# Kernel optimization log

Measured on AMD Instinct MI355X. Metric: run time of the kernel, lower is better.

Reference implementation:

```python
import jax, jax.numpy as jnp
import numpy as np

SORB = 64
S = SORB // 2          # 32 pair-sites
D = 64                 # d_model
H = 8                  # n_heads
L = 6                  # n_layers
ALPHA = 16
BETA = 16
NEG = -1e30


def _ln(x, g, b, eps=1e-5):
    m = jnp.mean(x, -1, keepdims=True)
    v = jnp.mean((x - m) ** 2, -1, keepdims=True)
    return (x - m) * jax.lax.rsqrt(v + eps) * g + b


def setup_inputs() -> dict:
    key = jax.random.key(0)
    ks = jax.random.split(key, 16)
    B = 8192
    # valid +/-1 configurations: exactly ALPHA ups (even cols) and BETA downs (odd cols)
    su = jax.random.uniform(ks[0], (B, S))
    sd = jax.random.uniform(ks[1], (B, S))
    thr_u = jnp.sort(su, 1)[:, ALPHA - 1:ALPHA]
    thr_d = jnp.sort(sd, 1)[:, BETA - 1:BETA]
    up = (su <= thr_u).astype(jnp.float32)
    dn = (sd <= thr_d).astype(jnp.float32)
    x = (jnp.stack([up, dn], -1).reshape(B, SORB) * 2.0 - 1.0).astype(jnp.float32)
    sc = 0.02
    inp = {
        'x': x,
        'tok_emb': jax.random.normal(ks[2], (5, D), jnp.float32) * sc,
        'pos_emb': jax.random.normal(ks[3], (S, D), jnp.float32) * sc,
        'ln1_g': jnp.ones((L, D), jnp.float32), 'ln1_b': jnp.zeros((L, D), jnp.float32),
        'wqkv': jax.random.normal(ks[4], (L, D, 3 * D), jnp.float32) * sc,
        'bqkv': jnp.zeros((L, 3 * D), jnp.float32),
        'wo': jax.random.normal(ks[5], (L, D, D), jnp.float32) * sc,
        'bo': jnp.zeros((L, D), jnp.float32),
        'ln2_g': jnp.ones((L, D), jnp.float32), 'ln2_b': jnp.zeros((L, D), jnp.float32),
        'w1': jax.random.normal(ks[6], (L, D, 4 * D), jnp.float32) * sc,
        'b1': jnp.zeros((L, 4 * D), jnp.float32),
        'w2': jax.random.normal(ks[7], (L, 4 * D, D), jnp.float32) * sc,
        'b2': jnp.zeros((L, D), jnp.float32),
        'lnf_g': jnp.ones((D,), jnp.float32), 'lnf_b': jnp.zeros((D,), jnp.float32),
        'w_out': jax.random.normal(ks[8], (D, 4), jnp.float32) * sc,
        'b_out': jnp.zeros((4,), jnp.float32),
        'wp1': jax.random.normal(ks[9], (SORB, 64), jnp.float32) * sc,
        'bp1': jnp.zeros((64,), jnp.float32),
        'wp2': jax.random.normal(ks[10], (64, 64), jnp.float32) * sc,
        'bp2': jnp.zeros((64,), jnp.float32),
        'wp3': jax.random.normal(ks[11], (64, 1), jnp.float32) * sc,
        'bp3': jnp.zeros((1,), jnp.float32),
    }
    return inp


def _forward(x, tok_emb, pos_emb, ln1_g, ln1_b, wqkv, bqkv, wo, bo, ln2_g, ln2_b,
             w1, b1, w2, b2, lnf_g, lnf_b, w_out, b_out, wp1, bp1, wp2, bp2, wp3, bp3):
    B = x.shape[0]
    xb = ((x + 1.0) * 0.5).astype(jnp.int32)          # 0/1 occupations
    u = xb[:, 0::2]                                   # [B,S] up occ per pair
    dn = xb[:, 1::2]                                  # [B,S] down occ per pair
    pair_idx = u + 2 * dn                             # state_to_int: 0..3
    # amp input: pad token 4 then first S-1 pair codes (teacher-forced decoder)
    tokens = jnp.concatenate([jnp.full((B, 1), 4, jnp.int32), pair_idx[:, :S - 1]], 1)
    h = tok_emb[tokens] + pos_emb[None, :, :]
    hd = D // H
    causal = jnp.tril(jnp.ones((S, S), bool))
    for l in range(L):
        a = _ln(h, ln1_g[l], ln1_b[l])
        qkv = a @ wqkv[l] + bqkv[l]
        q, k, v = jnp.split(qkv, 3, -1)
        q = q.reshape(B, S, H, hd); k = k.reshape(B, S, H, hd); v = v.reshape(B, S, H, hd)
        scores = jnp.einsum('bshd,bthd->bhst', q, k) / np.sqrt(hd).astype(np.float32)
        att = jax.nn.softmax(jnp.where(causal, scores, NEG), -1)
        o = jnp.einsum('bhst,bthd->bshd', att, v).reshape(B, S, D)
        h = h + o @ wo[l] + bo[l]
        a = _ln(h, ln2_g[l], ln2_b[l])
        h = h + jax.nn.relu(a @ w1[l] + b1[l]) @ w2[l] + b2[l]
    logits = _ln(h, lnf_g, lnf_b) @ w_out + b_out     # [B,S,4]
    # symmetry mask: Fock -> FCI space (particle-number constraints per spin)
    nup = jnp.cumsum(u, 1) - u                        # exclusive prefix counts
    ndn = jnp.cumsum(dn, 1) - dn
    rem = (S - 1) - jnp.arange(S)                     # pairs remaining after this one
    du = jnp.array([0, 1, 0, 1], jnp.int32)           # option order: empty, a, b, full
    dd = jnp.array([0, 0, 1, 1], jnp.int32)
    nu = nup[..., None] + du
    nd = ndn[..., None] + dd                          # [B,S,4]
    r = rem[None, :, None]
    mask = (nu <= ALPHA) & (nd <= BETA) & (ALPHA - nu <= r) & (BETA - nd <= r)
    lp = jax.nn.log_softmax(jnp.where(mask, logits, NEG), -1)
    amps_log = jnp.take_along_axis(lp, pair_idx[..., None], 2)[..., 0].sum(1)  # [B]
    # phase MLP on the raw +/-1 configuration
    ph = jax.nn.relu(x @ wp1 + bp1)
    ph = jax.nn.relu(ph @ wp2 + bp2)
    ph = (ph @ wp3 + bp3).reshape(-1)
    return jnp.exp(1j * ph) * jnp.exp(0.5 * amps_log)  # complex wavefunction [B]


def reference(x, tok_emb, pos_emb, ln1_g, ln1_b, wqkv, bqkv, wo, bo, ln2_g, ln2_b,
              w1, b1, w2, b2, lnf_g, lnf_b, w_out, b_out, wp1, bp1, wp2, bp2, wp3, bp3):
    return _forward(x, tok_emb, pos_emb, ln1_g, ln1_b, wqkv, bqkv, wo, bo, ln2_g, ln2_b,
                    w1, b1, w2, b2, lnf_g, lnf_b, w_out, b_out, wp1, bp1, wp2, bp2, wp3, bp3)
```

## Files before the change

kernel.cpp:

```cpp
#include <hip/hip_runtime.h>

#define NEGV -1e30f
#define STR 36

__device__ __forceinline__ float4 ld4(const float* p) {
  return *reinterpret_cast<const float4*>(p);
}

__device__ __forceinline__ void fma8(float (&acc)[8], float4 w0, float4 w1, float a) {
  acc[0] = fmaf(a, w0.x, acc[0]);
  acc[1] = fmaf(a, w0.y, acc[1]);
  acc[2] = fmaf(a, w0.z, acc[2]);
  acc[3] = fmaf(a, w0.w, acc[3]);
  acc[4] = fmaf(a, w1.x, acc[4]);
  acc[5] = fmaf(a, w1.y, acc[5]);
  acc[6] = fmaf(a, w1.z, acc[6]);
  acc[7] = fmaf(a, w1.w, acc[7]);
}

__launch_bounds__(256, 2)
__global__ void dwf_kernel(
    const float* __restrict__ x,
    const float* __restrict__ tok_emb,
    const float* __restrict__ pos_emb,
    const float* __restrict__ ln1_g, const float* __restrict__ ln1_b,
    const float* __restrict__ wqkv,  const float* __restrict__ bqkv,
    const float* __restrict__ wo,    const float* __restrict__ bo,
    const float* __restrict__ ln2_g, const float* __restrict__ ln2_b,
    const float* __restrict__ w1,    const float* __restrict__ b1,
    const float* __restrict__ w2,    const float* __restrict__ b2,
    const float* __restrict__ lnf_g, const float* __restrict__ lnf_b,
    const float* __restrict__ w_out, const float* __restrict__ b_out,
    const float* __restrict__ wp1,   const float* __restrict__ bp1,
    const float* __restrict__ wp2,   const float* __restrict__ bp2,
    const float* __restrict__ wp3,   const float* __restrict__ bp3,
    float* __restrict__ out, int out_pairs, int nB)
{
  const int s2   = blockIdx.x;
  const int tid  = threadIdx.x;
  const int w    = tid >> 6;
  const int lane = tid & 63;
  const int i32  = tid & 31;
  const int hh   = tid >> 5;
  const int g    = (tid >> 5) & 1;
  const bool valid1 = (2 * s2 + 1) < nB;

  __shared__ float SA0[64 * STR], SA1[64 * STR];
  __shared__ float SB0[64 * STR], SB1[64 * STR];
  __shared__ float xs[128], phb[128];
  __shared__ int   pis[64], toks[64];

  const float* xbase = x + s2 * 128;
  if (tid < 128) xs[tid] = (tid < 64 || valid1) ? xbase[tid] : 0.f;

  unsigned long long um = 0ull, dm = 0ull;
  if (w < 2) {
    int ub = 0, db = 0;
    if (lane < 32 && (w == 0 || valid1)) {
      const float* xr = xbase + 64 * w;
      ub = xr[2 * i32]     > 0.f;
      db = xr[2 * i32 + 1] > 0.f;
    }
    um = __ballot(ub);
    dm = __ballot(db);
    int pi   = ub + 2 * db;
    int prev = __shfl_up(pi, 1);
    if (lane < 32) {
      pis[32 * w + i32]  = pi;
      toks[32 * w + i32] = (i32 == 0) ? 4 : prev;
    }
  }
  __syncthreads();

  float h0[8], h1[8];
  #pragma unroll
  for (int q = 0; q < 8; ++q) {
    int r = 8 * w + q;
    float pe = pos_emb[r * 64 + lane];
    h0[q] = tok_emb[toks[r] * 64 + lane]      + pe;
    h1[q] = tok_emb[toks[32 + r] * 64 + lane] + pe;
  }

  auto layernorm2 = [&](const float* gp, const float* bp) {
    float gv = gp[lane], bv = bp[lane];
    float va[8], vb[8];
    #pragma unroll
    for (int q = 0; q < 8; ++q) {
      float sa = h0[q], qa_ = h0[q] * h0[q];
      float sb = h1[q], qb_ = h1[q] * h1[q];
      #pragma unroll
      for (int off = 32; off; off >>= 1) {
        sa  += __shfl_xor(sa, off);
        qa_ += __shfl_xor(qa_, off);
        sb  += __shfl_xor(sb, off);
        qb_ += __shfl_xor(qb_, off);
      }
      float ma = sa * 0.015625f, mb = sb * 0.015625f;
      float ra = rsqrtf(fmaf(-ma, ma, qa_ * 0.015625f) + 1e-5f);
      float rb = rsqrtf(fmaf(-mb, mb, qb_ * 0.015625f) + 1e-5f);
      va[q] = fmaf((h0[q] - ma) * ra, gv, bv);
      vb[q] = fmaf((h1[q] - mb) * rb, gv, bv);
    }
    *reinterpret_cast<float4*>(&SA0[lane * STR + 8 * w])     = make_float4(va[0], va[1], va[2], va[3]);
    *reinterpret_cast<float4*>(&SA0[lane * STR + 8 * w + 4]) = make_float4(va[4], va[5], va[6], va[7]);
    *reinterpret_cast<float4*>(&SA1[lane * STR + 8 * w])     = make_float4(vb[0], vb[1], vb[2], vb[3]);
    *reinterpret_cast<float4*>(&SA1[lane * STR + 8 * w + 4]) = make_float4(vb[4], vb[5], vb[6], vb[7]);
  };

  for (int l = 0; l < 6; ++l) {
    layernorm2(ln1_g + l * 64, ln1_b + l * 64);
    __syncthreads();

    const float* wl = wqkv + l * 64 * 192;
    const float* bq = bqkv + l * 192;
    float qa0[8], qa1[8];
    #pragma unroll
    for (int e = 0; e < 8; ++e) { qa0[e] = bq[8 * hh + e]; qa1[e] = qa0[e]; }
    float kb = bq[64 + lane], vbb = bq[128 + lane];
    float k0a[8], k1a[8], v0a[8], v1a[8];
    #pragma unroll
    for (int q = 0; q < 8; ++q) { k0a[q] = kb; k1a[q] = kb; v0a[q] = vbb; v1a[q] = vbb; }

    #pragma unroll 2
    for (int d = 0; d < 64; ++d) {
      const float* wr = wl + d * 192;
      float4 wq0 = ld4(wr + 8 * hh);
      float4 wq1 = ld4(wr + 8 * hh + 4);
      float  wk  = wr[64 + lane];
      float  wv  = wr[128 + lane];
      float  av0 = SA0[d * STR + i32];
      float  av1 = SA1[d * STR + i32];
      float4 a0l = ld4(&SA0[d * STR + 8 * w]);
      float4 a0h = ld4(&SA0[d * STR + 8 * w + 4]);
      float4 a1l = ld4(&SA1[d * STR + 8 * w]);
      float4 a1h = ld4(&SA1[d * STR + 8 * w + 4]);
      fma8(qa0, wq0, wq1, av0);
      fma8(qa1, wq0, wq1, av1);
      fma8(k0a, a0l, a0h, wk);
      fma8(k1a, a1l, a1h, wk);
      fma8(v0a, a0l, a0h, wv);
      fma8(v1a, a1l, a1h, wv);
    }
    #pragma unroll
    for (int e = 0; e < 8; ++e) {
      qa0[e] *= 0.35355339059327373f;
      qa1[e] *= 0.35355339059327373f;
    }
    __syncthreads();

    *reinterpret_cast<float4*>(&SA0[lane * STR + 8 * w])     = make_float4(k0a[0], k0a[1], k0a[2], k0a[3]);
    *reinterpret_cast<float4*>(&SA0[lane * STR + 8 * w + 4]) = make_float4(k0a[4], k0a[5], k0a[6], k0a[7]);
    *reinterpret_cast<float4*>(&SA1[lane * STR + 8 * w])     = make_float4(k1a[0], k1a[1], k1a[2], k1a[3]);
    *reinterpret_cast<float4*>(&SA1[lane * STR + 8 * w + 4]) = make_float4(k1a[4], k1a[5], k1a[6], k1a[7]);
    *reinterpret_cast<float4*>(&SB0[lane * STR + 8 * w])     = make_float4(v0a[0], v0a[1], v0a[2], v0a[3]);
    *reinterpret_cast<float4*>(&SB0[lane * STR + 8 * w + 4]) = make_float4(v0a[4], v0a[5], v0a[6], v0a[7]);
    *reinterpret_cast<float4*>(&SB1[lane * STR + 8 * w])     = make_float4(v1a[0], v1a[1], v1a[2], v1a[3]);
    *reinterpret_cast<float4*>(&SB1[lane * STR + 8 * w + 4]) = make_float4(v1a[4], v1a[5], v1a[6], v1a[7]);
    __syncthreads();

    {
      float p[32];
      #pragma unroll
      for (int j4 = 0; j4 < 8; ++j4) {
        float a0 = 0.f, a1 = 0.f, a2 = 0.f, a3 = 0.f;
        #pragma unroll
        for (int c = 0; c < 8; ++c) {
          float4 kv = ld4(&SA0[(8 * hh + c) * STR + 4 * j4]);
          a0 = fmaf(qa0[c], kv.x, a0);
          a1 = fmaf(qa0[c], kv.y, a1);
          a2 = fmaf(qa0[c], kv.z, a2);
          a3 = fmaf(qa0[c], kv.w, a3);
        }
        p[4 * j4]     = a0;
        p[4 * j4 + 1] = a1;
        p[4 * j4 + 2] = a2;
        p[4 * j4 + 3] = a3;
      }
      float mx = NEGV;
      #pragma unroll
      for (int j = 0; j < 32; ++j) {
        p[j] = (j <= i32) ? p[j] : NEGV;
        mx = fmaxf(mx, p[j]);
      }
      float sum = 0.f;
      #pragma unroll
      for (int j = 0; j < 32; ++j) {
        p[j] = __expf(p[j] - mx);
        sum += p[j];
      }
      float inv = 1.0f / sum;
      #pragma unroll
      for (int e = 0; e < 8; ++e) {
        float acc = 0.f;
        #pragma unroll
        for (int j4 = 0; j4 < 8; ++j4) {
          float4 vv = ld4(&SB0[(8 * hh + e) * STR + 4 * j4]);
          acc = fmaf(p[4 * j4],     vv.x, acc);
          acc = fmaf(p[4 * j4 + 1], vv.y, acc);
          acc = fmaf(p[4 * j4 + 2], vv.z, acc);
          acc = fmaf(p[4 * j4 + 3], vv.w, acc);
        }
        SA0[(8 * hh + e) * STR + i32] = acc * inv;
      }
    }
    {
      float p[32];
      #pragma unroll
      for (int j4 = 0; j4 < 8; ++j4) {
        float a0 = 0.f, a1 = 0.f, a2 = 0.f, a3 = 0.f;
        #pragma unroll
        for (int c = 0; c < 8; ++c) {
          float4 kv = ld4(&SA1[(8 * hh + c) * STR + 4 * j4]);
          a0 = fmaf(qa1[c], kv.x, a0);
          a1 = fmaf(qa1[c], kv.y, a1);
          a2 = fmaf(qa1[c], kv.z, a2);
          a3 = fmaf(qa1[c], kv.w, a3);
        }
        p[4 * j4]     = a0;
        p[4 * j4 + 1] = a1;
        p[4 * j4 + 2] = a2;
        p[4 * j4 + 3] = a3;
      }
      float mx = NEGV;
      #pragma unroll
      for (int j = 0; j < 32; ++j) {
        p[j] = (j <= i32) ? p[j] : NEGV;
        mx = fmaxf(mx, p[j]);
      }
      float sum = 0.f;
      #pragma unroll
      for (int j = 0; j < 32; ++j) {
        p[j] = __expf(p[j] - mx);
        sum += p[j];
      }
      float inv = 1.0f / sum;
      #pragma unroll
      for (int e = 0; e < 8; ++e) {
        float acc = 0.f;
        #pragma unroll
        for (int j4 = 0; j4 < 8; ++j4) {
          float4 vv = ld4(&SB1[(8 * hh + e) * STR + 4 * j4]);
          acc = fmaf(p[4 * j4],     vv.x, acc);
          acc = fmaf(p[4 * j4 + 1], vv.y, acc);
          acc = fmaf(p[4 * j4 + 2], vv.z, acc);
          acc = fmaf(p[4 * j4 + 3], vv.w, acc);
        }
        SA1[(8 * hh + e) * STR + i32] = acc * inv;
      }
    }
    __syncthreads();

    const float* wop = wo + l * 4096 + lane;
    #pragma unroll 2
    for (int d = 0; d < 64; ++d) {
      float wv = wop[d * 64];
      float4 o0l = ld4(&SA0[d * STR + 8 * w]);
      float4 o0h = ld4(&SA0[d * STR + 8 * w + 4]);
      float4 o1l = ld4(&SA1[d * STR + 8 * w]);
      float4 o1h = ld4(&SA1[d * STR + 8 * w + 4]);
      fma8(h0, o0l, o0h, wv);
      fma8(h1, o1l, o1h, wv);
    }
    {
      float bov = bo[l * 64 + lane];
      #pragma unroll
      for (int q = 0; q < 8; ++q) { h0[q] += bov; h1[q] += bov; }
    }

    layernorm2(ln2_g + l * 64, ln2_b + l * 64);
    const float* w1base = w1 + l * 64 * 256;
    const float* w2base = w2 + l * 256 * 64;
    for (int cc = 0; cc < 4; ++cc) {
      float b1v = b1[l * 256 + cc * 64 + lane];
      float m0[8], m1v[8];
      #pragma unroll
      for (int q = 0; q < 8; ++q) { m0[q] = b1v; m1v[q] = b1v; }
      const float* w1p = w1base + cc * 64 + lane;
      #pragma unroll 2
      for (int d = 0; d < 64; ++d) {
        float wv = w1p[d * 256];
        float4 a0l = ld4(&SA0[d * STR + 8 * w]);
        float4 a0h = ld4(&SA0[d * STR + 8 * w + 4]);
        float4 a1l = ld4(&SA1[d * STR + 8 * w]);
        float4 a1h = ld4(&SA1[d * STR + 8 * w + 4]);
        fma8(m0,  a0l, a0h, wv);
        fma8(m1v, a1l, a1h, wv);
      }
      *reinterpret_cast<float4*>(&SB0[lane * STR + 8 * w]) =
          make_float4(fmaxf(m0[0], 0.f), fmaxf(m0[1], 0.f),
                      fmaxf(m0[2], 0.f), fmaxf(m0[3], 0.f));
      *reinterpret_cast<float4*>(&SB0[lane * STR + 8 * w + 4]) =
          make_float4(fmaxf(m0[4], 0.f), fmaxf(m0[5], 0.f),
                      fmaxf(m0[6], 0.f), fmaxf(m0[7], 0.f));
      *reinterpret_cast<float4*>(&SB1[lane * STR + 8 * w]) =
          make_float4(fmaxf(m1v[0], 0.f), fmaxf(m1v[1], 0.f),
                      fmaxf(m1v[2], 0.f), fmaxf(m1v[3], 0.f));
      *reinterpret_cast<float4*>(&SB1[lane * STR + 8 * w + 4]) =
          make_float4(fmaxf(m1v[4], 0.f), fmaxf(m1v[5], 0.f),
                      fmaxf(m1v[6], 0.f), fmaxf(m1v[7], 0.f));
      const float* w2p = w2base + cc * 64 * 64 + lane;
      #pragma unroll 2
      for (int dc = 0; dc < 64; ++dc) {
        float wv = w2p[dc * 64];
        float4 q0l = ld4(&SB0[dc * STR + 8 * w]);
        float4 q0h = ld4(&SB0[dc * STR + 8 * w + 4]);
        float4 q1l = ld4(&SB1[dc * STR + 8 * w]);
        float4 q1h = ld4(&SB1[dc * STR + 8 * w + 4]);
        fma8(h0, q0l, q0h, wv);
        fma8(h1, q1l, q1h, wv);
      }
    }
    {
      float b2v = b2[l * 64 + lane];
      #pragma unroll
      for (int q = 0; q < 8; ++q) { h0[q] += b2v; h1[q] += b2v; }
    }
  }

  layernorm2(lnf_g, lnf_b);
  __syncthreads();

  if (w < 2) {
    const float* SAt = w ? SA1 : SA0;
    float la = b_out[2 * g], lb = b_out[2 * g + 1];
    #pragma unroll 4
    for (int d = 0; d < 64; ++d) {
      float av = SAt[d * STR + i32];
      la = fmaf(av, w_out[d * 4 + 2 * g],     la);
      lb = fmaf(av, w_out[d * 4 + 2 * g + 1], lb);
    }
    float lc  = __shfl_xor(la, 32);
    float ldt = __shfl_xor(lb, 32);

    int r   = i32;
    int nup = __popcll(um & ((1ull << r) - 1ull));
    int ndn = __popcll(dm & ((1ull << r) - 1ull));
    int rem = 31 - r;
    float lg[4] = {la, lb, lc, ldt};
    float ml[4];
    #pragma unroll
    for (int c = 0; c < 4; ++c) {
      int nu = nup + (c & 1);
      int nd = ndn + (c >> 1);
      bool ok = (nu <= 16) && (nd <= 16) && (16 - nu <= rem) && (16 - nd <= rem);
      ml[c] = ok ? lg[c] : NEGV;
    }
    float m4 = fmaxf(fmaxf(ml[0], ml[1]), fmaxf(ml[2], ml[3]));
    float se = __expf(ml[0] - m4) + __expf(ml[1] - m4) +
               __expf(ml[2] - m4) + __expf(ml[3] - m4);
    int c = pis[32 * w + r];
    float mls = (c == 0) ? ml[0] : (c == 1) ? ml[1] : (c == 2) ? ml[2] : ml[3];
    float amps = (lane < 32) ? (mls - m4 - __logf(se)) : 0.f;
    #pragma unroll
    for (int off = 32; off; off >>= 1) amps += __shfl_xor(amps, off);

    const float* xst = xs + 64 * w;
    float p1 = bp1[lane];
    #pragma unroll 4
    for (int d = 0; d < 64; ++d)
      p1 = fmaf(xst[d], wp1[d * 64 + lane], p1);
    p1 = fmaxf(p1, 0.f);
    phb[64 * w + lane] = p1;
    float p2 = bp2[lane];
    #pragma unroll 4
    for (int d = 0; d < 64; ++d)
      p2 = fmaf(phb[64 * w + d], wp2[d * 64 + lane], p2);
    p2 = fmaxf(p2, 0.f);
    float p3 = p2 * wp3[lane];
    #pragma unroll
    for (int off = 32; off; off >>= 1) p3 += __shfl_xor(p3, off);
    float ph = p3 + bp3[0];

    if (lane == 0 && (w == 0 || valid1)) {
      int S = 2 * s2 + w;
      float amp = expf(0.5f * amps);
      if (out_pairs) {
        out[2 * S]     = amp * cosf(ph);
        out[2 * S + 1] = amp * sinf(ph);
      } else {
        out[S] = amp * cosf(ph);
      }
    }
  }
}

extern "C" void kernel_launch(void* const* d_in, const int* in_sizes, int n_in,
                              void* d_out, int out_size, void* d_ws, size_t ws_size,
                              hipStream_t stream) {
  (void)n_in; (void)d_ws; (void)ws_size;
  const int B = in_sizes[0] / 64;
  const int out_pairs = (out_size >= 2 * B) ? 1 : 0;
  const int grid = (B + 1) / 2;
  dwf_kernel<<<grid, 256, 0, stream>>>(
      (const float*)d_in[0],  (const float*)d_in[1],  (const float*)d_in[2],
      (const float*)d_in[3],  (const float*)d_in[4],  (const float*)d_in[5],
      (const float*)d_in[6],  (const float*)d_in[7],  (const float*)d_in[8],
      (const float*)d_in[9],  (const float*)d_in[10], (const float*)d_in[11],
      (const float*)d_in[12], (const float*)d_in[13], (const float*)d_in[14],
      (const float*)d_in[15], (const float*)d_in[16], (const float*)d_in[17],
      (const float*)d_in[18], (const float*)d_in[19], (const float*)d_in[20],
      (const float*)d_in[21], (const float*)d_in[22], (const float*)d_in[23],
      (const float*)d_in[24], (float*)d_out, out_pairs, B);
}
```

Measured before the change: 2.951 ms.

## Software-pipeline weight loads in GEMM loops and pair FFN chunk computation

Rewrites the QKV, output-projection, FFN1 and FFN2 inner loops so that global weight loads for the next group of rows are issued into double-buffered registers before the current group's FMAs run. This hides global-memory latency behind LDS reads and arithmetic. The FFN1 loop now computes two hidden chunks at once, so each shared-memory activation load is reused twice. The cost is higher register pressure, which under launch_bounds(256,2) could cause spills.

```diff
diff --git a/kernel.cpp b/kernel.cpp
--- a/kernel.cpp
+++ b/kernel.cpp
@@ -107,6 +107,40 @@
     *reinterpret_cast<float4*>(&SA1[lane * STR + 8 * w + 4]) = make_float4(vb[4], vb[5], vb[6], vb[7]);
   };
 
+  auto w2pass = [&](const float* w2p) {
+    float gA[8], gB[8];
+    #pragma unroll
+    for (int u = 0; u < 8; ++u) gA[u] = w2p[u * 64];
+    #pragma unroll 1
+    for (int dp = 0; dp < 4; ++dp) {
+      const int ds = dp * 16;
+      #pragma unroll
+      for (int u = 0; u < 8; ++u) gB[u] = w2p[((ds + 8 + u) & 63) * 64];
+      #pragma unroll
+      for (int u = 0; u < 8; ++u) {
+        const int dc = ds + u;
+        float4 q0l = ld4(&SB0[dc * STR + 8 * w]);
+        float4 q0h = ld4(&SB0[dc * STR + 8 * w + 4]);
+        float4 q1l = ld4(&SB1[dc * STR + 8 * w]);
+        float4 q1h = ld4(&SB1[dc * STR + 8 * w + 4]);
+        fma8(h0, q0l, q0h, gA[u]);
+        fma8(h1, q1l, q1h, gA[u]);
+      }
+      #pragma unroll
+      for (int u = 0; u < 8; ++u) gA[u] = w2p[((ds + 16 + u) & 63) * 64];
+      #pragma unroll
+      for (int u = 0; u < 8; ++u) {
+        const int dc = ds + 8 + u;
+        float4 q0l = ld4(&SB0[dc * STR + 8 * w]);
+        float4 q0h = ld4(&SB0[dc * STR + 8 * w + 4]);
+        float4 q1l = ld4(&SB1[dc * STR + 8 * w]);
+        float4 q1h = ld4(&SB1[dc * STR + 8 * w + 4]);
+        fma8(h0, q0l, q0h, gB[u]);
+        fma8(h1, q1l, q1h, gB[u]);
+      }
+    }
+  };
+
   for (int l = 0; l < 6; ++l) {
     layernorm2(ln1_g + l * 64, ln1_b + l * 64);
     __syncthreads();
@@ -121,25 +155,62 @@
     #pragma unroll
     for (int q = 0; q < 8; ++q) { k0a[q] = kb; k1a[q] = kb; v0a[q] = vbb; v1a[q] = vbb; }
 
-    #pragma unroll 2
-    for (int d = 0; d < 64; ++d) {
-      const float* wr = wl + d * 192;
-      float4 wq0 = ld4(wr + 8 * hh);
-      float4 wq1 = ld4(wr + 8 * hh + 4);
-      float  wk  = wr[64 + lane];
-      float  wv  = wr[128 + lane];
-      float  av0 = SA0[d * STR + i32];
-      float  av1 = SA1[d * STR + i32];
-      float4 a0l = ld4(&SA0[d * STR + 8 * w]);
-      float4 a0h = ld4(&SA0[d * STR + 8 * w + 4]);
-      float4 a1l = ld4(&SA1[d * STR + 8 * w]);
-      float4 a1h = ld4(&SA1[d * STR + 8 * w + 4]);
-      fma8(qa0, wq0, wq1, av0);
-      fma8(qa1, wq0, wq1, av1);
-      fma8(k0a, a0l, a0h, wk);
-      fma8(k1a, a1l, a1h, wk);
-      fma8(v0a, a0l, a0h, wv);
-      fma8(v1a, a1l, a1h, wv);
+    const float* wkp = wl + 64 + lane;
+    const float* wvp = wl + 128 + lane;
+    float kwA[4], vwA[4], kwB[4], vwB[4];
+    #pragma unroll
+    for (int u = 0; u < 4; ++u) { kwA[u] = wkp[u * 192]; vwA[u] = wvp[u * 192]; }
+    #pragma unroll 1
+    for (int dp = 0; dp < 8; ++dp) {
+      const int ds = dp * 8;
+      #pragma unroll
+      for (int u = 0; u < 4; ++u) {
+        const int dn = (ds + 4 + u) & 63;
+        kwB[u] = wkp[dn * 192]; vwB[u] = wvp[dn * 192];
+      }
+      #pragma unroll
+      for (int u = 0; u < 4; ++u) {
+        const int d = ds + u;
+        const float* wr = wl + d * 192;
+        float4 wq0 = ld4(wr + 8 * hh);
+        float4 wq1 = ld4(wr + 8 * hh + 4);
+        float  av0 = SA0[d * STR + i32];
+        float  av1 = SA1[d * STR + i32];
+        float4 a0l = ld4(&SA0[d * STR + 8 * w]);
+        float4 a0h = ld4(&SA0[d * STR + 8 * w + 4]);
+        float4 a1l = ld4(&SA1[d * STR + 8 * w]);
+        float4 a1h = ld4(&SA1[d * STR + 8 * w + 4]);
+        fma8(qa0, wq0, wq1, av0);
+        fma8(qa1, wq0, wq1, av1);
+        fma8(k0a, a0l, a0h, kwA[u]);
+        fma8(k1a, a1l, a1h, kwA[u]);
+        fma8(v0a, a0l, a0h, vwA[u]);
+        fma8(v1a, a1l, a1h, vwA[u]);
+      }
+      #pragma unroll
+      for (int u = 0; u < 4; ++u) {
+        const int dn = (ds + 8 + u) & 63;
+        kwA[u] = wkp[dn * 192]; vwA[u] = wvp[dn * 192];
+      }
+      #pragma unroll
+      for (int u = 0; u < 4; ++u) {
+        const int d = ds + 4 + u;
+        const float* wr = wl + d * 192;
+        float4 wq0 = ld4(wr + 8 * hh);
+        float4 wq1 = ld4(wr + 8 * hh + 4);
+        float  av0 = SA0[d * STR + i32];
+        float  av1 = SA1[d * STR + i32];
+        float4 a0l = ld4(&SA0[d * STR + 8 * w]);
+        float4 a0h = ld4(&SA0[d * STR + 8 * w + 4]);
+        float4 a1l = ld4(&SA1[d * STR + 8 * w]);
+        float4 a1h = ld4(&SA1[d * STR + 8 * w + 4]);
+        fma8(qa0, wq0, wq1, av0);
+        fma8(qa1, wq0, wq1, av1);
+        fma8(k0a, a0l, a0h, kwB[u]);
+        fma8(k1a, a1l, a1h, kwB[u]);
+        fma8(v0a, a0l, a0h, vwB[u]);
+        fma8(v1a, a1l, a1h, vwB[u]);
+      }
     }
     #pragma unroll
     for (int e = 0; e < 8; ++e) {
@@ -250,18 +321,39 @@
     }
     __syncthreads();
 
-    const float* wop = wo + l * 4096 + lane;
-    #pragma unroll 2
-    for (int d = 0; d < 64; ++d) {
-      float wv = wop[d * 64];
-      float4 o0l = ld4(&SA0[d * STR + 8 * w]);
-      float4 o0h = ld4(&SA0[d * STR + 8 * w + 4]);
-      float4 o1l = ld4(&SA1[d * STR + 8 * w]);
-      float4 o1h = ld4(&SA1[d * STR + 8 * w + 4]);
-      fma8(h0, o0l, o0h, wv);
-      fma8(h1, o1l, o1h, wv);
-    }
     {
+      const float* wop = wo + l * 4096 + lane;
+      float owA[8], owB[8];
+      #pragma unroll
+      for (int u = 0; u < 8; ++u) owA[u] = wop[u * 64];
+      #pragma unroll 1
+      for (int dp = 0; dp < 4; ++dp) {
+        const int ds = dp * 16;
+        #pragma unroll
+        for (int u = 0; u < 8; ++u) owB[u] = wop[((ds + 8 + u) & 63) * 64];
+        #pragma unroll
+        for (int u = 0; u < 8; ++u) {
+          const int d = ds + u;
+          float4 o0l = ld4(&SA0[d * STR + 8 * w]);
+          float4 o0h = ld4(&SA0[d * STR + 8 * w + 4]);
+          float4 o1l = ld4(&SA1[d * STR + 8 * w]);
+          float4 o1h = ld4(&SA1[d * STR + 8 * w + 4]);
+          fma8(h0, o0l, o0h, owA[u]);
+          fma8(h1, o1l, o1h, owA[u]);
+        }
+        #pragma unroll
+        for (int u = 0; u < 8; ++u) owA[u] = wop[((ds + 16 + u) & 63) * 64];
+        #pragma unroll
+        for (int u = 0; u < 8; ++u) {
+          const int d = ds + 8 + u;
+          float4 o0l = ld4(&SA0[d * STR + 8 * w]);
+          float4 o0h = ld4(&SA0[d * STR + 8 * w + 4]);
+          float4 o1l = ld4(&SA1[d * STR + 8 * w]);
+          float4 o1h = ld4(&SA1[d * STR + 8 * w + 4]);
+          fma8(h0, o0l, o0h, owB[u]);
+          fma8(h1, o1l, o1h, owB[u]);
+        }
+      }
       float bov = bo[l * 64 + lane];
       #pragma unroll
       for (int q = 0; q < 8; ++q) { h0[q] += bov; h1[q] += bov; }
@@ -270,45 +362,85 @@
     layernorm2(ln2_g + l * 64, ln2_b + l * 64);
     const float* w1base = w1 + l * 64 * 256;
     const float* w2base = w2 + l * 256 * 64;
-    for (int cc = 0; cc < 4; ++cc) {
-      float b1v = b1[l * 256 + cc * 64 + lane];
-      float m0[8], m1v[8];
-      #pragma unroll
-      for (int q = 0; q < 8; ++q) { m0[q] = b1v; m1v[q] = b1v; }
-      const float* w1p = w1base + cc * 64 + lane;
-      #pragma unroll 2
-      for (int d = 0; d < 64; ++d) {
-        float wv = w1p[d * 256];
-        float4 a0l = ld4(&SA0[d * STR + 8 * w]);
-        float4 a0h = ld4(&SA0[d * STR + 8 * w + 4]);
-        float4 a1l = ld4(&SA1[d * STR + 8 * w]);
-        float4 a1h = ld4(&SA1[d * STR + 8 * w + 4]);
-        fma8(m0,  a0l, a0h, wv);
-        fma8(m1v, a1l, a1h, wv);
+    #pragma unroll 1
+    for (int ccp = 0; ccp < 2; ++ccp) {
+      const int ccA = 2 * ccp, ccB = ccA + 1;
+      float mA0[8], mA1[8], mB0[8], mB1[8];
+      {
+        float bA = b1[l * 256 + ccA * 64 + lane];
+        float bB = b1[l * 256 + ccB * 64 + lane];
+        #pragma unroll
+        for (int q = 0; q < 8; ++q) { mA0[q] = bA; mA1[q] = bA; mB0[q] = bB; mB1[q] = bB; }
+      }
+      const float* wpA = w1base + ccA * 64 + lane;
+      const float* wpB = w1base + ccB * 64 + lane;
+      float fA1[4], fB1[4], fA2[4], fB2[4];
+      #pragma unroll
+      for (int u = 0; u < 4; ++u) { fA1[u] = wpA[u * 256]; fB1[u] = wpB[u * 256]; }
+      #pragma unroll 1
+      for (int dp = 0; dp < 8; ++dp) {
+        const int ds = dp * 8;
+        #pragma unroll
+        for (int u = 0; u < 4; ++u) {
+          const int dn = (ds + 4 + u) & 63;
+          fA2[u] = wpA[dn * 256]; fB2[u] = wpB[dn * 256];
+        }
+        #pragma unroll
+        for (int u = 0; u < 4; ++u) {
+          const int d = ds + u;
+          float4 a0l = ld4(&SA0[d * STR + 8 * w]);
+          float4 a0h = ld4(&SA0[d * STR + 8 * w + 4]);
+          float4 a1l = ld4(&SA1[d * STR + 8 * w]);
+          float4 a1h = ld4(&SA1[d * STR + 8 * w + 4]);
+          fma8(mA0, a0l, a0h, fA1[u]);
+          fma8(mA1, a1l, a1h, fA1[u]);
+          fma8(mB0, a0l, a0h, fB1[u]);
+          fma8(mB1, a1l, a1h, fB1[u]);
+        }
+        #pragma unroll
+        for (int u = 0; u < 4; ++u) {
+          const int dn = (ds + 8 + u) & 63;
+          fA1[u] = wpA[dn * 256]; fB1[u] = wpB[dn * 256];
+        }
+        #pragma unroll
+        for (int u = 0; u < 4; ++u) {
+          const int d = ds + 4 + u;
+          float4 a0l = ld4(&SA0[d * STR + 8 * w]);
+          float4 a0h = ld4(&SA0[d * STR + 8 * w + 4]);
+          float4 a1l = ld4(&SA1[d * STR + 8 * w]);
+          float4 a1h = ld4(&SA1[d * STR + 8 * w + 4]);
+          fma8(mA0, a0l, a0h, fA2[u]);
+          fma8(mA1, a1l, a1h, fA2[u]);
+          fma8(mB0, a0l, a0h, fB2[u]);
+          fma8(mB1, a1l, a1h, fB2[u]);
+        }
       }
       *reinterpret_cast<float4*>(&SB0[lane * STR + 8 * w]) =
-          make_float4(fmaxf(m0[0], 0.f), fmaxf(m0[1], 0.f),
-                      fmaxf(m0[2], 0.f), fmaxf(m0[3], 0.f));
+          make_float4(fmaxf(mA0[0], 0.f), fmaxf(mA0[1], 0.f),
+                      fmaxf(mA0[2], 0.f), fmaxf(mA0[3], 0.f));
       *reinterpret_cast<float4*>(&SB0[lane * STR + 8 * w + 4]) =
-          make_float4(fmaxf(m0[4], 0.f), fmaxf(m0[5], 0.f),
-                      fmaxf(m0[6], 0.f), fmaxf(m0[7], 0.f));
+          make_float4(fmaxf(mA0[4], 0.f), fmaxf(mA0[5], 0.f),
+                      fmaxf(mA0[6], 0.f), fmaxf(mA0[7], 0.f));
       *reinterpret_cast<float4*>(&SB1[lane * STR + 8 * w]) =
-          make_float4(fmaxf(m1v[0], 0.f), fmaxf(m1v[1], 0.f),
-                      fmaxf(m1v[2], 0.f), fmaxf(m1v[3], 0.f));
+          make_float4(fmaxf(mA1[0], 0.f), fmaxf(mA1[1], 0.f),
+                      fmaxf(mA1[2], 0.f), fmaxf(mA1[3], 0.f));
       *reinterpret_cast<float4*>(&SB1[lane * STR + 8 * w + 4]) =
-          make_float4(fmaxf(m1v[4], 0.f), fmaxf(m1v[5], 0.f),
-                      fmaxf(m1v[6], 0.f), fmaxf(m1v[7], 0.f));
-      const float* w2p = w2base + cc * 64 * 64 + lane;
-      #pragma unroll 2
-      for (int dc = 0; dc < 64; ++dc) {
-        float wv = w2p[dc * 64];
-        float4 q0l = ld4(&SB0[dc * STR + 8 * w]);
-        float4 q0h = ld4(&SB0[dc * STR + 8 * w + 4]);
-        float4 q1l = ld4(&SB1[dc * STR + 8 * w]);
-        float4 q1h = ld4(&SB1[dc * STR + 8 * w + 4]);
-        fma8(h0, q0l, q0h, wv);
-        fma8(h1, q1l, q1h, wv);
-      }
+          make_float4(fmaxf(mA1[4], 0.f), fmaxf(mA1[5], 0.f),
+                      fmaxf(mA1[6], 0.f), fmaxf(mA1[7], 0.f));
+      w2pass(w2base + ccA * 64 * 64 + lane);
+      *reinterpret_cast<float4*>(&SB0[lane * STR + 8 * w]) =
+          make_float4(fmaxf(mB0[0], 0.f), fmaxf(mB0[1], 0.f),
+                      fmaxf(mB0[2], 0.f), fmaxf(mB0[3], 0.f));
+      *reinterpret_cast<float4*>(&SB0[lane * STR + 8 * w + 4]) =
+          make_float4(fmaxf(mB0[4], 0.f), fmaxf(mB0[5], 0.f),
+                      fmaxf(mB0[6], 0.f), fmaxf(mB0[7], 0.f));
+      *reinterpret_cast<float4*>(&SB1[lane * STR + 8 * w]) =
+          make_float4(fmaxf(mB1[0], 0.f), fmaxf(mB1[1], 0.f),
+                      fmaxf(mB1[2], 0.f), fmaxf(mB1[3], 0.f));
+      *reinterpret_cast<float4*>(&SB1[lane * STR + 8 * w + 4]) =
+          make_float4(fmaxf(mB1[4], 0.f), fmaxf(mB1[5], 0.f),
+                      fmaxf(mB1[6], 0.f), fmaxf(mB1[7], 0.f));
+      w2pass(w2base + ccB * 64 * 64 + lane);
     }
     {
       float b2v = b2[l * 64 + lane];
```

Result: faster. 2.734 ms (median of 2 runs) (-7.4%).
